# Optimization experiments

Hardware: AMD Instinct MI355X
Metric: run time of the kernel (lower is better)

The kernel has to match this reference:

```python
import jax, jax.numpy as jnp
import numpy as np

N_NODES = 100000
N_EDGES = 1600000
D_IN = 128
D_HID = 128
D_OUT = 128


def _sage_conv(x, src, dst, W_l, b_l, W_r, num_nodes):
    # PyG SAGEConv (aggr='mean'): out = lin_l(mean_{j in N(i)} x_j) + lin_r(x_i)
    msg = x[src]  # [E, d] gather source features
    agg = jax.ops.segment_sum(msg, dst, num_segments=num_nodes)  # [N, d]
    deg = jax.ops.segment_sum(jnp.ones((src.shape[0],), x.dtype), dst, num_segments=num_nodes)
    mean = agg / jnp.maximum(deg, 1.0)[:, None]
    return mean @ W_l.T + b_l + x @ W_r.T


def setup_inputs() -> dict:
    key = jax.random.key(0)
    ks = jax.random.split(key, 8)
    x = jax.random.normal(ks[0], (N_NODES, D_IN), dtype=jnp.float32)
    edge_index = jax.random.randint(ks[1], (2, N_EDGES), 0, N_NODES, dtype=jnp.int64)
    s = 1.0 / np.sqrt(D_IN)
    W_l1 = jax.random.uniform(ks[2], (D_HID, D_IN), jnp.float32, -s, s)
    b_l1 = jnp.zeros((D_HID,), jnp.float32)
    W_r1 = jax.random.uniform(ks[3], (D_HID, D_IN), jnp.float32, -s, s)
    s2 = 1.0 / np.sqrt(D_HID)
    W_l2 = jax.random.uniform(ks[4], (D_OUT, D_HID), jnp.float32, -s2, s2)
    b_l2 = jnp.zeros((D_OUT,), jnp.float32)
    W_r2 = jax.random.uniform(ks[5], (D_OUT, D_HID), jnp.float32, -s2, s2)
    return {"x": x, "edge_index": edge_index, "W_l1": W_l1, "b_l1": b_l1,
            "W_r1": W_r1, "W_l2": W_l2, "b_l2": b_l2, "W_r2": W_r2}


def reference(x, edge_index, W_l1, b_l1, W_r1, W_l2, b_l2, W_r2):
    src, dst = edge_index[0], edge_index[1]
    n = x.shape[0]
    h = _sage_conv(x, src, dst, W_l1, b_l1, W_r1, n)
    h = jax.nn.relu(h)
    out = _sage_conv(h, src, dst, W_l2, b_l2, W_r2, n)
    return out
```

## Files before the change

kernel.cpp:

```cpp
#include <hip/hip_runtime.h>
#include <stdint.h>

typedef short bf16x8 __attribute__((ext_vector_type(8)));
typedef unsigned short u16x8 __attribute__((ext_vector_type(8)));
typedef float f32x4 __attribute__((ext_vector_type(4)));

#define NPB 512
#define BSHIFT 9
#define MAXBUCK 256
#define STAGE_CAP 12288
#define LROW 136
#define BINWIN 8192

__device__ __forceinline__ short f2bf(float f) {
    uint32_t u = __float_as_uint(f);
    u += 0x7fffu + ((u >> 16) & 1u);
    return (short)(u >> 16);
}
__device__ __forceinline__ float bf2f(unsigned short s) {
    return __uint_as_float((uint32_t)s << 16);
}

__global__ __launch_bounds__(256) void prep_kernel(
    const float* __restrict__ x, short* __restrict__ xb, int nx,
    const float* __restrict__ w0, const float* __restrict__ w1,
    const float* __restrict__ w2, const float* __restrict__ w3,
    short* __restrict__ o0, short* __restrict__ o1,
    short* __restrict__ o2, short* __restrict__ o3,
    const int* __restrict__ dst, int* __restrict__ bcnt, int E, int B,
    int cxBlocks, int histBlocks)
{
    int b = blockIdx.x;
    if (b < cxBlocks) {
        int i = (b * 256 + threadIdx.x) * 8;
        if (i + 8 <= nx) {
            const float4 v0 = *(const float4*)(x + i);
            const float4 v1 = *(const float4*)(x + i + 4);
            bf16x8 o;
            o[0] = f2bf(v0.x); o[1] = f2bf(v0.y); o[2] = f2bf(v0.z); o[3] = f2bf(v0.w);
            o[4] = f2bf(v1.x); o[5] = f2bf(v1.y); o[6] = f2bf(v1.z); o[7] = f2bf(v1.w);
            *(bf16x8*)(xb + i) = o;
        } else {
            for (int j = i; j < nx; ++j) xb[j] = f2bf(x[j]);
        }
        return;
    }
    b -= cxBlocks;
    if (b < 64) {
        int i = b * 256 + threadIdx.x;
        o0[i] = f2bf(w0[i]);
        o1[i] = f2bf(w1[i]);
        o2[i] = f2bf(w2[i]);
        o3[i] = f2bf(w3[i]);
        return;
    }
    b -= 64;
    __shared__ int h[MAXBUCK];
    for (int i = threadIdx.x; i < B; i += 256) h[i] = 0;
    __syncthreads();
    const int stride = histBlocks * 256;
    for (int e = b * 256 + threadIdx.x; e < E; e += stride)
        atomicAdd(&h[dst[e] >> BSHIFT], 1);
    __syncthreads();
    for (int i = threadIdx.x; i < B; i += 256)
        if (h[i]) atomicAdd(&bcnt[i], h[i]);
}

__global__ __launch_bounds__(256) void bscan_kernel(const int* __restrict__ bcnt,
                                                    int* __restrict__ bbase,
                                                    int* __restrict__ gcur,
                                                    int* __restrict__ rowptr,
                                                    int E, int N, int B) {
    __shared__ int s[256];
    int t = threadIdx.x;
    int v = (t < B) ? bcnt[t] : 0;
    s[t] = v;
    __syncthreads();
    for (int off = 1; off < 256; off <<= 1) {
        int a = (t >= off) ? s[t - off] : 0;
        __syncthreads();
        s[t] += a;
        __syncthreads();
    }
    int excl = s[t] - v;
    if (t < B) { bbase[t] = excl; gcur[t] = excl; }
    if (t == B - 1) bbase[B] = excl + v;
    if (t == 0) rowptr[N] = E;
}

__global__ __launch_bounds__(512) void bin_kernel(const int* __restrict__ src,
                                                  const int* __restrict__ dst,
                                                  int* __restrict__ gcur,
                                                  unsigned int* __restrict__ binned,
                                                  int E, int B) {
    __shared__ int cnt[MAXBUCK];
    __shared__ int base[MAXBUCK];
    for (int i = threadIdx.x; i < B; i += 512) cnt[i] = 0;
    __syncthreads();
    const int e0 = blockIdx.x * BINWIN;
    const int eEnd = (e0 + BINWIN < E) ? (e0 + BINWIN) : E;
#pragma unroll 4
    for (int e = e0 + threadIdx.x; e < eEnd; e += 512)
        atomicAdd(&cnt[dst[e] >> BSHIFT], 1);
    __syncthreads();
    for (int i = threadIdx.x; i < B; i += 512) {
        int c = cnt[i];
        base[i] = c ? atomicAdd(&gcur[i], c) : 0;
        cnt[i] = 0;
    }
    __syncthreads();
#pragma unroll 4
    for (int e = e0 + threadIdx.x; e < eEnd; e += 512) {
        int sv = src[e], dv = dst[e];
        int b = dv >> BSHIFT;
        int off = atomicAdd(&cnt[b], 1);
        binned[base[b] + off] = ((unsigned)sv << BSHIFT) | (unsigned)(dv & (NPB - 1));
    }
}

__global__ __launch_bounds__(512) void build_kernel(const unsigned int* __restrict__ binned,
                                                    const int* __restrict__ bbase,
                                                    int* __restrict__ rowptr,
                                                    int* __restrict__ csr, int N) {
    __shared__ int hist[NPB];
    __shared__ int cur[NPB];
    __shared__ int scanb[NPB];
    __shared__ int stage[STAGE_CAP];
    const int b = blockIdx.x;
    const int t = threadIdx.x;
    const int cbeg = bbase[b], cend = bbase[b + 1];
    const int cnt = cend - cbeg;
    hist[t] = 0;
    __syncthreads();
    for (int i = t; i < cnt; i += 512)
        atomicAdd(&hist[binned[cbeg + i] & (NPB - 1)], 1);
    __syncthreads();
    const int ps = hist[t];
    scanb[t] = ps;
    __syncthreads();
    for (int off = 1; off < 512; off <<= 1) {
        int a = (t >= off) ? scanb[t - off] : 0;
        __syncthreads();
        scanb[t] += a;
        __syncthreads();
    }
    const int e0 = scanb[t] - ps;
    cur[t] = e0;
    const int node = (b << BSHIFT) + t;
    if (node < N) rowptr[node] = cbeg + e0;
    __syncthreads();
    for (int i = t; i < cnt; i += 512) {
        unsigned rec = binned[cbeg + i];
        int ld  = rec & (NPB - 1);
        int pos = atomicAdd(&cur[ld], 1);
        if (pos < STAGE_CAP) stage[pos] = (int)(rec >> BSHIFT);
        else                 csr[cbeg + pos] = (int)(rec >> BSHIFT);
    }
    __syncthreads();
    const int lim = cnt < STAGE_CAP ? cnt : STAGE_CAP;
    for (int i = t; i < lim; i += 512)
        csr[cbeg + i] = stage[i];
}

#define ACC8(u) do { \
    a0 += bf2f(u[0]); a1 += bf2f(u[1]); a2 += bf2f(u[2]); a3 += bf2f(u[3]); \
    a4 += bf2f(u[4]); a5 += bf2f(u[5]); a6 += bf2f(u[6]); a7 += bf2f(u[7]); } while (0)

template <bool RELU>
__global__ __launch_bounds__(256) void fused_kernel(
    const short* __restrict__ feat, const int* __restrict__ csr,
    const int* __restrict__ rowptr,
    const short* __restrict__ Wl, const short* __restrict__ Wr,
    const float* __restrict__ bias,
    short* __restrict__ outb, float* __restrict__ outf, int N)
{
    __shared__ short lmean[32 * LROW];
    const int lane = threadIdx.x & 63;
    const int wave = threadIdx.x >> 6;
    const int q    = lane >> 4;
    const int ql   = lane & 15;
    const int nb0  = blockIdx.x * 32;
    const int m0w  = nb0 + wave * 8;

    for (int it = 0; it < 2; ++it) {
        const int node = m0w + it * 4 + q;
        const int lrow = wave * 8 + it * 4 + q;
        float a0=0,a1=0,a2=0,a3=0,a4=0,a5=0,a6=0,a7=0;
        if (node < N) {
            const int beg = rowptr[node], end = rowptr[node + 1];
            int e = beg;
            for (; e + 4 <= end; e += 4) {
                const int s0 = csr[e], s1 = csr[e+1], s2 = csr[e+2], s3 = csr[e+3];
                const u16x8 u0 = *(const u16x8*)(feat + (size_t)s0 * 128 + ql * 8);
                const u16x8 u1 = *(const u16x8*)(feat + (size_t)s1 * 128 + ql * 8);
                const u16x8 u2 = *(const u16x8*)(feat + (size_t)s2 * 128 + ql * 8);
                const u16x8 u3 = *(const u16x8*)(feat + (size_t)s3 * 128 + ql * 8);
                ACC8(u0); ACC8(u1); ACC8(u2); ACC8(u3);
            }
            for (; e < end; ++e) {
                const u16x8 u = *(const u16x8*)(feat + (size_t)csr[e] * 128 + ql * 8);
                ACC8(u);
            }
            const float r = 1.0f / fmaxf((float)(end - beg), 1.0f);
            bf16x8 o;
            o[0] = f2bf(a0 * r); o[1] = f2bf(a1 * r); o[2] = f2bf(a2 * r); o[3] = f2bf(a3 * r);
            o[4] = f2bf(a4 * r); o[5] = f2bf(a5 * r); o[6] = f2bf(a6 * r); o[7] = f2bf(a7 * r);
            *(bf16x8*)(lmean + (size_t)lrow * LROW + ql * 8) = o;
        } else {
            *(bf16x8*)(lmean + (size_t)lrow * LROW + ql * 8) = (bf16x8)0;
        }
    }
    __syncthreads();

    const int t2 = wave >> 1;
    const int h  = wave & 1;
    const int m0 = nb0 + t2 * 16;
    f32x4 acc[4];
#pragma unroll
    for (int i = 0; i < 4; ++i) acc[i] = (f32x4)0.0f;
    const bool valid = (m0 + ql < N);

#pragma unroll
    for (int kk = 0; kk < 4; ++kk) {
        const int kb = kk * 32 + q * 8;
        const bf16x8 a = *(const bf16x8*)(lmean + (size_t)(t2 * 16 + ql) * LROW + kb);
#pragma unroll
        for (int nt = 0; nt < 4; ++nt) {
            const bf16x8 b = *(const bf16x8*)(Wl + (size_t)(h * 64 + nt * 16 + ql) * 128 + kb);
            acc[nt] = __builtin_amdgcn_mfma_f32_16x16x32_bf16(a, b, acc[nt], 0, 0, 0);
        }
    }
#pragma unroll
    for (int kk = 0; kk < 4; ++kk) {
        const int kb = kk * 32 + q * 8;
        bf16x8 a = (bf16x8)0;
        if (valid) a = *(const bf16x8*)(feat + (size_t)(m0 + ql) * 128 + kb);
#pragma unroll
        for (int nt = 0; nt < 4; ++nt) {
            const bf16x8 b = *(const bf16x8*)(Wr + (size_t)(h * 64 + nt * 16 + ql) * 128 + kb);
            acc[nt] = __builtin_amdgcn_mfma_f32_16x16x32_bf16(a, b, acc[nt], 0, 0, 0);
        }
    }

    const int rbase = m0 + q * 4;
#pragma unroll
    for (int nt = 0; nt < 4; ++nt) {
        const int col = h * 64 + nt * 16 + ql;
        const float bc = bias[col];
#pragma unroll
        for (int r = 0; r < 4; ++r) {
            const int node = rbase + r;
            if (node < N) {
                float v = acc[nt][r] + bc;
                if (RELU) outb[(size_t)node * 128 + col] = f2bf(fmaxf(v, 0.0f));
                else      outf[(size_t)node * 128 + col] = v;
            }
        }
    }
}

extern "C" void kernel_launch(void* const* d_in, const int* in_sizes, int n_in,
                              void* d_out, int out_size, void* d_ws, size_t ws_size,
                              hipStream_t stream) {
    const float* x   = (const float*)d_in[0];
    const int*   ei  = (const int*)d_in[1];
    const float* Wl1 = (const float*)d_in[2];
    const float* bl1 = (const float*)d_in[3];
    const float* Wr1 = (const float*)d_in[4];
    const float* Wl2 = (const float*)d_in[5];
    const float* bl2 = (const float*)d_in[6];
    const float* Wr2 = (const float*)d_in[7];

    const int N = in_sizes[0] / 128;
    const int E = in_sizes[1] / 2;
    const int* src = ei;
    const int* dst = ei + E;
    const int B = (N + NPB - 1) >> BSHIFT;

    char* wsb = (char*)d_ws;
    short* hbuf = (short*)wsb;
    size_t off = (size_t)N * 128 * 2;
    short* wl1 = (short*)(wsb + off); off += 16384 * 2;
    short* wr1 = (short*)(wsb + off); off += 16384 * 2;
    short* wl2 = (short*)(wsb + off); off += 16384 * 2;
    short* wr2 = (short*)(wsb + off); off += 16384 * 2;
    int* rowptr = (int*)(wsb + off);
    off += ((size_t)(N + 1) * 4 + 15) & ~(size_t)15;
    int* csr = (int*)(wsb + off);
    off += ((size_t)E * 4 + 15) & ~(size_t)15;
    unsigned int* binned = (unsigned int*)(wsb + off);
    off += ((size_t)E * 4 + 15) & ~(size_t)15;
    int* bcnt  = (int*)(wsb + off);
    int* bbase = bcnt + (MAXBUCK + 1);
    int* gcur  = bbase + (MAXBUCK + 1);

    short* xb  = (short*)d_out;
    float* out = (float*)d_out;

    const int nx = N * 128;
    const int cxBlocks    = (nx / 8 + 255) / 256;
    const int histBlocks  = 1024;
    const int binBlocks   = (E + BINWIN - 1) / BINWIN;
    const int fusedBlocks = (N + 31) / 32;

    (void)hipMemsetAsync(bcnt, 0, (size_t)(MAXBUCK + 1) * sizeof(int), stream);

    prep_kernel<<<cxBlocks + 64 + histBlocks, 256, 0, stream>>>(
        x, xb, nx, Wl1, Wr1, Wl2, Wr2, wl1, wr1, wl2, wr2,
        dst, bcnt, E, B, cxBlocks, histBlocks);
    bscan_kernel<<<1, 256, 0, stream>>>(bcnt, bbase, gcur, rowptr, E, N, B);
    bin_kernel<<<binBlocks, 512, 0, stream>>>(src, dst, gcur, binned, E, B);
    build_kernel<<<B, 512, 0, stream>>>(binned, bbase, rowptr, csr, N);

    fused_kernel<true><<<fusedBlocks, 256, 0, stream>>>(xb, csr, rowptr, wl1, wr1, bl1,
                                                        hbuf, (float*)nullptr, N);
    fused_kernel<false><<<fusedBlocks, 256, 0, stream>>>(hbuf, csr, rowptr, wl2, wr2, bl2,
                                                         (short*)nullptr, out, N);
}
```

Measured before the change: 418.9 us.

## Merge CSR build pipeline into one persistent kernel with grid barriers

Replaces the four preprocessing launches (prep, bucket scan, binning, per-bucket CSR build) with a single kernel of B blocks that uses atomic-counter grid barriers between phases. It aims to remove launch gaps and the tail effects between the small kernels. The trade-off is that only B (about 196) blocks of 512 threads now do the bf16 conversion and histogram, which may lower parallelism compared with the thousands of blocks used before. The barriers also depend on all blocks being co-resident.

```diff
diff --git a/kernel.cpp b/kernel.cpp
--- a/kernel.cpp
+++ b/kernel.cpp
@@ -10,7 +10,6 @@
 #define MAXBUCK 256
 #define STAGE_CAP 12288
 #define LROW 136
-#define BINWIN 8192
 
 __device__ __forceinline__ short f2bf(float f) {
     uint32_t u = __float_as_uint(f);
@@ -21,145 +20,146 @@
     return __uint_as_float((uint32_t)s << 16);
 }
 
-__global__ __launch_bounds__(256) void prep_kernel(
+__device__ __forceinline__ void gbar(int* bar, int idx, int G) {
+    __syncthreads();
+    if (threadIdx.x == 0) {
+        __threadfence();
+        atomicAdd(&bar[idx], 1);
+        while (atomicAdd(&bar[idx], 0) < G) __builtin_amdgcn_s_sleep(8);
+    }
+    __syncthreads();
+    __threadfence();
+}
+
+__global__ __launch_bounds__(512) void chain_kernel(
     const float* __restrict__ x, short* __restrict__ xb, int nx,
     const float* __restrict__ w0, const float* __restrict__ w1,
     const float* __restrict__ w2, const float* __restrict__ w3,
     short* __restrict__ o0, short* __restrict__ o1,
     short* __restrict__ o2, short* __restrict__ o3,
-    const int* __restrict__ dst, int* __restrict__ bcnt, int E, int B,
-    int cxBlocks, int histBlocks)
+    const int* __restrict__ src, const int* __restrict__ dst,
+    int* __restrict__ bcnt, int* __restrict__ bbase,
+    int* __restrict__ gcur, int* __restrict__ bar,
+    unsigned int* __restrict__ binned,
+    int* __restrict__ rowptr, int* __restrict__ csr,
+    int E, int N, int B, int G, int win)
 {
-    int b = blockIdx.x;
-    if (b < cxBlocks) {
-        int i = (b * 256 + threadIdx.x) * 8;
-        if (i + 8 <= nx) {
-            const float4 v0 = *(const float4*)(x + i);
-            const float4 v1 = *(const float4*)(x + i + 4);
+    __shared__ int sh[3 * NPB + STAGE_CAP];
+    const int t = threadIdx.x;
+    const int g = blockIdx.x;
+    const int stride = G * 512;
+
+    {
+        int* h = sh;
+        for (int i = t; i < B; i += 512) h[i] = 0;
+        __syncthreads();
+        for (int i = g * 512 + t; i < 16384; i += stride) {
+            o0[i] = f2bf(w0[i]);
+            o1[i] = f2bf(w1[i]);
+            o2[i] = f2bf(w2[i]);
+            o3[i] = f2bf(w3[i]);
+        }
+        const int ncx = nx >> 3;
+        for (int i = g * 512 + t; i < ncx; i += stride) {
+            const int j = i << 3;
+            const float4 v0 = *(const float4*)(x + j);
+            const float4 v1 = *(const float4*)(x + j + 4);
             bf16x8 o;
             o[0] = f2bf(v0.x); o[1] = f2bf(v0.y); o[2] = f2bf(v0.z); o[3] = f2bf(v0.w);
             o[4] = f2bf(v1.x); o[5] = f2bf(v1.y); o[6] = f2bf(v1.z); o[7] = f2bf(v1.w);
-            *(bf16x8*)(xb + i) = o;
-        } else {
-            for (int j = i; j < nx; ++j) xb[j] = f2bf(x[j]);
-        }
-        return;
-    }
-    b -= cxBlocks;
-    if (b < 64) {
-        int i = b * 256 + threadIdx.x;
-        o0[i] = f2bf(w0[i]);
-        o1[i] = f2bf(w1[i]);
-        o2[i] = f2bf(w2[i]);
-        o3[i] = f2bf(w3[i]);
-        return;
-    }
-    b -= 64;
-    __shared__ int h[MAXBUCK];
-    for (int i = threadIdx.x; i < B; i += 256) h[i] = 0;
-    __syncthreads();
-    const int stride = histBlocks * 256;
-    for (int e = b * 256 + threadIdx.x; e < E; e += stride)
-        atomicAdd(&h[dst[e] >> BSHIFT], 1);
-    __syncthreads();
-    for (int i = threadIdx.x; i < B; i += 256)
-        if (h[i]) atomicAdd(&bcnt[i], h[i]);
-}
-
-__global__ __launch_bounds__(256) void bscan_kernel(const int* __restrict__ bcnt,
-                                                    int* __restrict__ bbase,
-                                                    int* __restrict__ gcur,
-                                                    int* __restrict__ rowptr,
-                                                    int E, int N, int B) {
-    __shared__ int s[256];
-    int t = threadIdx.x;
-    int v = (t < B) ? bcnt[t] : 0;
-    s[t] = v;
-    __syncthreads();
-    for (int off = 1; off < 256; off <<= 1) {
-        int a = (t >= off) ? s[t - off] : 0;
-        __syncthreads();
-        s[t] += a;
-        __syncthreads();
-    }
-    int excl = s[t] - v;
-    if (t < B) { bbase[t] = excl; gcur[t] = excl; }
-    if (t == B - 1) bbase[B] = excl + v;
-    if (t == 0) rowptr[N] = E;
-}
-
-__global__ __launch_bounds__(512) void bin_kernel(const int* __restrict__ src,
-                                                  const int* __restrict__ dst,
-                                                  int* __restrict__ gcur,
-                                                  unsigned int* __restrict__ binned,
-                                                  int E, int B) {
-    __shared__ int cnt[MAXBUCK];
-    __shared__ int base[MAXBUCK];
-    for (int i = threadIdx.x; i < B; i += 512) cnt[i] = 0;
-    __syncthreads();
-    const int e0 = blockIdx.x * BINWIN;
-    const int eEnd = (e0 + BINWIN < E) ? (e0 + BINWIN) : E;
+            *(bf16x8*)(xb + j) = o;
+        }
+        for (int e = g * 512 + t; e < E; e += stride)
+            atomicAdd(&h[dst[e] >> BSHIFT], 1);
+        __syncthreads();
+        for (int i = t; i < B; i += 512)
+            if (h[i]) atomicAdd(&bcnt[i], h[i]);
+    }
+    gbar(bar, 0, G);
+
+    if (g == 0) {
+        int* s = sh;
+        const int v = (t < B) ? atomicAdd(&bcnt[t], 0) : 0;
+        s[t] = v;
+        __syncthreads();
+        for (int off = 1; off < 512; off <<= 1) {
+            int a = (t >= off) ? s[t - off] : 0;
+            __syncthreads();
+            s[t] += a;
+            __syncthreads();
+        }
+        const int excl = s[t] - v;
+        if (t < B) { bbase[t] = excl; gcur[t] = excl; }
+        if (t == B - 1) bbase[B] = excl + v;
+        if (t == 0) rowptr[N] = E;
+    }
+    gbar(bar, 1, G);
+
+    {
+        int* cnt  = sh;
+        int* base = sh + MAXBUCK;
+        for (int i = t; i < B; i += 512) cnt[i] = 0;
+        __syncthreads();
+        const int e0 = g * win;
+        const int eEnd = (e0 + win < E) ? (e0 + win) : E;
 #pragma unroll 4
-    for (int e = e0 + threadIdx.x; e < eEnd; e += 512)
-        atomicAdd(&cnt[dst[e] >> BSHIFT], 1);
-    __syncthreads();
-    for (int i = threadIdx.x; i < B; i += 512) {
-        int c = cnt[i];
-        base[i] = c ? atomicAdd(&gcur[i], c) : 0;
-        cnt[i] = 0;
-    }
-    __syncthreads();
+        for (int e = e0 + t; e < eEnd; e += 512)
+            atomicAdd(&cnt[dst[e] >> BSHIFT], 1);
+        __syncthreads();
+        for (int i = t; i < B; i += 512) {
+            int c = cnt[i];
+            base[i] = c ? atomicAdd(&gcur[i], c) : 0;
+            cnt[i] = 0;
+        }
+        __syncthreads();
 #pragma unroll 4
-    for (int e = e0 + threadIdx.x; e < eEnd; e += 512) {
-        int sv = src[e], dv = dst[e];
-        int b = dv >> BSHIFT;
-        int off = atomicAdd(&cnt[b], 1);
-        binned[base[b] + off] = ((unsigned)sv << BSHIFT) | (unsigned)(dv & (NPB - 1));
-    }
-}
-
-__global__ __launch_bounds__(512) void build_kernel(const unsigned int* __restrict__ binned,
-                                                    const int* __restrict__ bbase,
-                                                    int* __restrict__ rowptr,
-                                                    int* __restrict__ csr, int N) {
-    __shared__ int hist[NPB];
-    __shared__ int cur[NPB];
-    __shared__ int scanb[NPB];
-    __shared__ int stage[STAGE_CAP];
-    const int b = blockIdx.x;
-    const int t = threadIdx.x;
-    const int cbeg = bbase[b], cend = bbase[b + 1];
-    const int cnt = cend - cbeg;
-    hist[t] = 0;
-    __syncthreads();
-    for (int i = t; i < cnt; i += 512)
-        atomicAdd(&hist[binned[cbeg + i] & (NPB - 1)], 1);
-    __syncthreads();
-    const int ps = hist[t];
-    scanb[t] = ps;
-    __syncthreads();
-    for (int off = 1; off < 512; off <<= 1) {
-        int a = (t >= off) ? scanb[t - off] : 0;
-        __syncthreads();
-        scanb[t] += a;
-        __syncthreads();
-    }
-    const int e0 = scanb[t] - ps;
-    cur[t] = e0;
-    const int node = (b << BSHIFT) + t;
-    if (node < N) rowptr[node] = cbeg + e0;
-    __syncthreads();
-    for (int i = t; i < cnt; i += 512) {
-        unsigned rec = binned[cbeg + i];
-        int ld  = rec & (NPB - 1);
-        int pos = atomicAdd(&cur[ld], 1);
-        if (pos < STAGE_CAP) stage[pos] = (int)(rec >> BSHIFT);
-        else                 csr[cbeg + pos] = (int)(rec >> BSHIFT);
-    }
-    __syncthreads();
-    const int lim = cnt < STAGE_CAP ? cnt : STAGE_CAP;
-    for (int i = t; i < lim; i += 512)
-        csr[cbeg + i] = stage[i];
+        for (int e = e0 + t; e < eEnd; e += 512) {
+            int sv = src[e], dv = dst[e];
+            int b = dv >> BSHIFT;
+            int off = atomicAdd(&cnt[b], 1);
+            binned[base[b] + off] = ((unsigned)sv << BSHIFT) | (unsigned)(dv & (NPB - 1));
+        }
+    }
+    gbar(bar, 2, G);
+
+    if (g < B) {
+        int* hist  = sh;
+        int* cur   = sh + NPB;
+        int* scanb = sh + 2 * NPB;
+        int* stage = sh + 3 * NPB;
+        const int cbeg = bbase[g], cend = bbase[g + 1];
+        const int cnt = cend - cbeg;
+        hist[t] = 0;
+        __syncthreads();
+        for (int i = t; i < cnt; i += 512)
+            atomicAdd(&hist[binned[cbeg + i] & (NPB - 1)], 1);
+        __syncthreads();
+        const int ps = hist[t];
+        scanb[t] = ps;
+        __syncthreads();
+        for (int off = 1; off < 512; off <<= 1) {
+            int a = (t >= off) ? scanb[t - off] : 0;
+            __syncthreads();
+            scanb[t] += a;
+            __syncthreads();
+        }
+        const int e0 = scanb[t] - ps;
+        cur[t] = e0;
+        const int node = (g << BSHIFT) + t;
+        if (node < N) rowptr[node] = cbeg + e0;
+        __syncthreads();
+        for (int i = t; i < cnt; i += 512) {
+            unsigned rec = binned[cbeg + i];
+            int ld  = rec & (NPB - 1);
+            int pos = atomicAdd(&cur[ld], 1);
+            if (pos < STAGE_CAP) stage[pos] = (int)(rec >> BSHIFT);
+            else                 csr[cbeg + pos] = (int)(rec >> BSHIFT);
+        }
+        __syncthreads();
+        const int lim = cnt < STAGE_CAP ? cnt : STAGE_CAP;
+        for (int i = t; i < lim; i += 512)
+            csr[cbeg + i] = stage[i];
+    }
 }
 
 #define ACC8(u) do { \
@@ -285,32 +285,30 @@
     short* wl2 = (short*)(wsb + off); off += 16384 * 2;
     short* wr2 = (short*)(wsb + off); off += 16384 * 2;
     int* rowptr = (int*)(wsb + off);
-    off += ((size_t)(N + 1) * 4 + 15) & ~(size_t)15;
+    off += ((size_t)(N + 1) * 4 + 127) & ~(size_t)127;
     int* csr = (int*)(wsb + off);
-    off += ((size_t)E * 4 + 15) & ~(size_t)15;
+    off += ((size_t)E * 4 + 127) & ~(size_t)127;
     unsigned int* binned = (unsigned int*)(wsb + off);
-    off += ((size_t)E * 4 + 15) & ~(size_t)15;
+    off += ((size_t)E * 4 + 127) & ~(size_t)127;
     int* bcnt  = (int*)(wsb + off);
-    int* bbase = bcnt + (MAXBUCK + 1);
-    int* gcur  = bbase + (MAXBUCK + 1);
+    int* bbase = bcnt + 288;
+    int* gcur  = bbase + 288;
+    int* bar   = gcur + 256;
 
     short* xb  = (short*)d_out;
     float* out = (float*)d_out;
 
     const int nx = N * 128;
-    const int cxBlocks    = (nx / 8 + 255) / 256;
-    const int histBlocks  = 1024;
-    const int binBlocks   = (E + BINWIN - 1) / BINWIN;
+    const int G  = B;
+    const int win = (E + G - 1) / G;
     const int fusedBlocks = (N + 31) / 32;
 
-    (void)hipMemsetAsync(bcnt, 0, (size_t)(MAXBUCK + 1) * sizeof(int), stream);
-
-    prep_kernel<<<cxBlocks + 64 + histBlocks, 256, 0, stream>>>(
+    (void)hipMemsetAsync(bcnt, 0, (size_t)(288 + 288 + 256 + 32) * sizeof(int), stream);
+
+    chain_kernel<<<G, 512, 0, stream>>>(
         x, xb, nx, Wl1, Wr1, Wl2, Wr2, wl1, wr1, wl2, wr2,
-        dst, bcnt, E, B, cxBlocks, histBlocks);
-    bscan_kernel<<<1, 256, 0, stream>>>(bcnt, bbase, gcur, rowptr, E, N, B);
-    bin_kernel<<<binBlocks, 512, 0, stream>>>(src, dst, gcur, binned, E, B);
-    build_kernel<<<B, 512, 0, stream>>>(binned, bbase, rowptr, csr, N);
+        src, dst, bcnt, bbase, gcur, bar, binned, rowptr, csr,
+        E, N, B, G, win);
 
     fused_kernel<true><<<fusedBlocks, 256, 0, stream>>>(xb, csr, rowptr, wl1, wr1, bl1,
                                                         hbuf, (float*)nullptr, N);
```

Result: slower. 498.0 us (+18.9%).
